# Kernel tuning notes

Measured on AMD Instinct MI355X. Metric: run time of the kernel, lower is better.

Reference implementation:

```python
import jax, jax.numpy as jnp
import numpy as np

B, S, D, H = 4, 2048, 1024, 16
DK = D // H
THETA = 10000.0


def setup_inputs() -> dict:
    key = jax.random.key(0)
    ks = jax.random.split(key, 5)
    std = (2.0 / (D + D)) ** 0.5  # Linear init std (distribution differs from trunc-normal; math identical)
    x = jax.random.normal(ks[0], (B, S, D), dtype=jnp.float32)
    wq = jax.random.normal(ks[1], (D, D), dtype=jnp.float32) * std
    wk = jax.random.normal(ks[2], (D, D), dtype=jnp.float32) * std
    wv = jax.random.normal(ks[3], (D, D), dtype=jnp.float32) * std
    wo = jax.random.normal(ks[4], (D, D), dtype=jnp.float32) * std
    mask = jnp.tril(jnp.ones((S, S), dtype=bool))  # causal
    return {"x": x, "mask": mask, "wq": wq, "wk": wk, "wv": wv, "wo": wo}


def _rope(t):
    # t: [b, h, s, dk]; interleaved pairs (even, odd)
    s = t.shape[-2]
    inv_freq = THETA ** (-jnp.arange(0, DK, 2, dtype=jnp.float32) / DK)  # [dk/2]
    ang = jnp.arange(s, dtype=jnp.float32)[:, None] * inv_freq[None, :]  # [s, dk/2]
    cos = jnp.cos(ang)[None, None, :, :]
    sin = jnp.sin(ang)[None, None, :, :]
    x1 = t[..., 0::2]
    x2 = t[..., 1::2]
    rot = jnp.stack([x1 * cos - x2 * sin, x1 * sin + x2 * cos], axis=-1)
    return rot.reshape(t.shape)


def reference(x, mask, wq, wk, wv, wo):
    b, s, d = x.shape
    def heads(w):
        return jnp.einsum('bsd,ed->bse', x, w).reshape(b, s, H, DK).transpose(0, 2, 1, 3)
    q = _rope(heads(wq))
    k = _rope(heads(wk))
    v = heads(wv)
    scores = jnp.einsum('bhqd,bhkd->bhqk', q, k) / (DK ** 0.5)
    scores = jnp.where(mask, scores, -jnp.inf)
    attn = jax.nn.softmax(scores, axis=-1)
    out = jnp.einsum('bhqk,bhkd->bhqd', attn, v)
    out = out.transpose(0, 2, 1, 3).reshape(b, s, d)
    return jnp.einsum('bsd,ed->bse', out, wo)
```

## Files before the change

kernel.cpp:

```cpp
#include <hip/hip_runtime.h>

constexpr int Bc = 4, Sc = 2048, Dc = 1024, Hc = 16, DKc = 64;
constexpr int Mc = Bc * Sc;

typedef __bf16 bf16x8 __attribute__((ext_vector_type(8)));
typedef float f32x4 __attribute__((ext_vector_type(4)));
typedef unsigned short ush;

#define DEVI __device__ __forceinline__

DEVI ush bf(float f) { return __builtin_bit_cast(ush, (__bf16)f); }

DEVI void ld_lds16(const void* g, void* l) {
    __builtin_amdgcn_global_load_lds(
        (const __attribute__((address_space(1))) unsigned int*)g,
        (__attribute__((address_space(3))) unsigned int*)l,
        16, 0, 0);
}

constexpr unsigned CVT_BLOCKS = 6144;
constexpr unsigned TAB_BLOCKS = 32;

__global__ __launch_bounds__(256) void cvt_all(
    const float* __restrict__ x,  const float* __restrict__ wq,
    const float* __restrict__ wk, const float* __restrict__ wv,
    const float* __restrict__ wo, ush* __restrict__ dst,
    float2* __restrict__ csn)
{
    if (blockIdx.x >= CVT_BLOCKS) {
        int t = (int)(blockIdx.x - CVT_BLOCKS) * 256 + threadIdx.x;
#pragma unroll
        for (int i = 0; i < 8; i++) {
            int idx = t * 8 + i;
            int s = idx >> 5, p = idx & 31;
            float ang = (float)s * exp2f(-(float)p * 0.4152410118609203f);
            csn[idx] = make_float2(cosf(ang), sinf(ang));
        }
        return;
    }
    size_t t = ((size_t)blockIdx.x * 256 + threadIdx.x) * 8;
    const float* src; size_t loc;
    const size_t NX = (size_t)Mc * Dc;
    if (t < NX) { src = x; loc = t; }
    else {
        size_t u = t - NX;
        int wi = (int)(u >> 20);
        src = (wi == 0) ? wq : ((wi == 1) ? wk : ((wi == 2) ? wv : wo));
        loc = u & 1048575u;
    }
    float4 a = *(const float4*)(src + loc);
    float4 b = *(const float4*)(src + loc + 4);
    union { ush u[8]; float4 v; } o;
    o.u[0] = bf(a.x); o.u[1] = bf(a.y); o.u[2] = bf(a.z); o.u[3] = bf(a.w);
    o.u[4] = bf(b.x); o.u[5] = bf(b.y); o.u[6] = bf(b.z); o.u[7] = bf(b.w);
    *(float4*)(dst + t) = o.v;
}

template<int MODE>
__global__ __launch_bounds__(512, 4) void gemm_bf(
    const ush* __restrict__ A,
    const ush* __restrict__ W0, const ush* __restrict__ W1,
    const ush* __restrict__ W2,
    ush* __restrict__ Oq, ush* __restrict__ Ok, ush* __restrict__ Ovt,
    float* __restrict__ Of, const float2* __restrict__ csn)
{
    __shared__ ush sA[128 * 64];
    __shared__ ush sB[128 * 64];

    const int xcd = (int)blockIdx.x;
    const int u = (int)blockIdx.y + 64 * (int)blockIdx.z;
    const int z = (MODE == 0) ? (u >> 6) : 0;
    const int w = u & 63;
    const int m0 = (xcd * 8 + (w >> 3)) * 128;
    const int n0 = (w & 7) * 128;

    const ush* W = (z == 0) ? W0 : ((z == 1) ? W1 : W2);

    const int tid = threadIdx.x;
    const int wv = tid >> 6;
    const int ln = tid & 63;
    const int lr = ln & 15;
    const int lq = ln >> 4;
    const int wm = (wv & 1) * 64;
    const int wn = (wv >> 1) * 32;
    const int rL = ln >> 3;
    const int cSw = ((ln & 7) ^ rL) * 8;
    const int ca0 = lq ^ (ln & 7);

    f32x4 acc[4][2] = {};
    const bool swp = (MODE == 0) && (z == 2);

    for (int kt = 0; kt < 1024; kt += 64) {
        __syncthreads();
#pragma unroll
        for (int i = 0; i < 2; i++) {
            int chunk = wv * 2 + i;
            int rr = chunk * 8 + rL;
            ld_lds16(&A[(size_t)(m0 + rr) * 1024 + kt + cSw], &sA[chunk * 512]);
            ld_lds16(&W[(size_t)(n0 + rr) * 1024 + kt + cSw], &sB[chunk * 512]);
        }
        __syncthreads();
#pragma unroll
        for (int ks = 0; ks < 2; ks++) {
            const int cf = (ca0 ^ (ks << 2)) << 3;
            bf16x8 af[4], bfr[2];
#pragma unroll
            for (int t = 0; t < 4; t++)
                af[t]  = *(const bf16x8*)(&sA[(wm + t * 16 + lr) * 64 + cf]);
#pragma unroll
            for (int t = 0; t < 2; t++)
                bfr[t] = *(const bf16x8*)(&sB[(wn + t * 16 + lr) * 64 + cf]);
            __builtin_amdgcn_s_setprio(1);
            if (!swp) {
#pragma unroll
                for (int ia = 0; ia < 4; ia++)
#pragma unroll
                    for (int ib = 0; ib < 2; ib++)
                        acc[ia][ib] = __builtin_amdgcn_mfma_f32_16x16x32_bf16(
                            af[ia], bfr[ib], acc[ia][ib], 0, 0, 0);
            } else {
#pragma unroll
                for (int ia = 0; ia < 4; ia++)
#pragma unroll
                    for (int ib = 0; ib < 2; ib++)
                        acc[ia][ib] = __builtin_amdgcn_mfma_f32_16x16x32_bf16(
                            bfr[ib], af[ia], acc[ia][ib], 0, 0, 0);
            }
            __builtin_amdgcn_s_setprio(0);
        }
    }

    ush* Oqk = (z == 0) ? Oq : Ok;
#pragma unroll
    for (int ia = 0; ia < 4; ia++) {
#pragma unroll
        for (int ib = 0; ib < 2; ib++) {
#pragma unroll
            for (int r = 0; r < 4; r++) {
                float v = acc[ia][ib][r];
                if (MODE == 1) {
                    int m = m0 + wm + ia * 16 + lq * 4 + r;
                    int n = n0 + wn + ib * 16 + lr;
                    Of[(size_t)m * 1024 + n] = v;
                } else if (swp) {
                    int n = n0 + wn + ib * 16 + lq * 4 + r;
                    int m = m0 + wm + ia * 16 + lr;
                    Ovt[((size_t)((m >> 11) * Hc + (n >> 6)) * DKc + (n & 63)) * Sc
                        + (m & (Sc - 1))] = bf(v);
                } else {
                    int m = m0 + wm + ia * 16 + lq * 4 + r;
                    int n = n0 + wn + ib * 16 + lr;
                    float part = __shfl_xor(v, 1);
                    int dk = n & 63, s = m & (Sc - 1);
                    float2 cs = csn[(s << 5) + (dk >> 1)];
                    float res = (dk & 1) ? (part * cs.y + v * cs.x)
                                         : (v * cs.x - part * cs.y);
                    if (z == 0) res *= 0.18033688011112042f;
                    Oqk[((size_t)((m >> 11) * Hc + (n >> 6)) * Sc + s) * DKc + dk] = bf(res);
                }
            }
        }
    }
}

__global__ __launch_bounds__(512, 4) void attn_k(
    const ush* __restrict__ Q, const ush* __restrict__ Kr,
    const ush* __restrict__ Vt, ush* __restrict__ O)
{
    __shared__ ush kbuf[2][64 * 64];
    __shared__ ush vbuf[2][64 * 64];
    __shared__ ush pbuf[8][16 * 76];

    const int head = (int)blockIdx.x * 8 + ((int)blockIdx.y >> 3);
    const int qp   = (int)blockIdx.y & 7;
    const int tid = threadIdx.x;
    const int wv = tid >> 6;
    const int ln = tid & 63;
    const int lr = ln & 15;
    const int lq = ln >> 4;
    const size_t hoff = (size_t)head * Sc * DKc;
    const int rS = tid >> 3;
    const int c8 = tid & 7;
    const int cS = c8 * 8;
    const int cW = ((c8 ^ (rS & 7)) * 8);
    const int cw0 = ((lq ^ (lr & 7)) * 8);

#define BARRIER() { asm volatile("s_waitcnt lgkmcnt(0)" ::: "memory");       \
        __builtin_amdgcn_sched_barrier(0);                                   \
        __builtin_amdgcn_s_barrier(); }

#define LOADKV(ktv, kk, vv) {                                                \
        int kb_ = (ktv) * 64;                                                \
        kk = *(const float4*)(&Kr[hoff + (size_t)(kb_ + rS) * DKc + cS]);    \
        vv = *(const float4*)(&Vt[hoff + (size_t)rS * Sc + kb_ + cS]); }

#define WRITEKV(bb, kk, vv) {                                                \
        *(float4*)(&kbuf[bb][rS * 64 + cW]) = kk;                            \
        *(float4*)(&vbuf[bb][rS * 64 + cW]) = vv; }

#define COMPUTE(bb, ktv) {                                                   \
        const int kb = (ktv) * 64;                                           \
        f32x4 sc[4];                                                         \
        __builtin_amdgcn_s_setprio(1);                                       \
        _Pragma("unroll")                                                    \
        for (int nt = 0; nt < 4; nt++) {                                     \
            const ush* kr_ = &kbuf[bb][(nt * 16 + lr) * 64];                 \
            bf16x8 bk0 = *(const bf16x8*)(kr_ + cw0);                        \
            bf16x8 bk1 = *(const bf16x8*)(kr_ + (cw0 ^ 32));                 \
            f32x4 cc = {};                                                   \
            cc = __builtin_amdgcn_mfma_f32_16x16x32_bf16(aq0, bk0, cc, 0, 0, 0); \
            cc = __builtin_amdgcn_mfma_f32_16x16x32_bf16(aq1, bk1, cc, 0, 0, 0); \
            sc[nt] = cc;                                                     \
        }                                                                    \
        __builtin_amdgcn_s_setprio(0);                                       \
        const int rowq = qbase + wv * 16 + lq * 4;                           \
        const bool needmask = (kb + 63 > qbase + wv * 16);                   \
        _Pragma("unroll")                                                    \
        for (int nt = 0; nt < 4; nt++) {                                     \
            int col = kb + nt * 16 + lr;                                     \
            _Pragma("unroll")                                                \
            for (int r = 0; r < 4; r++) {                                    \
                float v = sc[nt][r];                                         \
                if (needmask && col > rowq + r) v = -1e30f;                  \
                float p = exp2f(v);                                          \
                sc[nt][r] = p;                                               \
                rs[r] += p;                                                  \
            }                                                                \
        }                                                                    \
        {                                                                    \
            ush* pb = pbuf[wv];                                              \
            _Pragma("unroll")                                                \
            for (int nt = 0; nt < 4; nt++)                                   \
                _Pragma("unroll")                                            \
                for (int r = 0; r < 4; r++)                                  \
                    pb[(lq * 4 + r) * 76 + nt * 16 + lr] = bf(sc[nt][r]);    \
            __builtin_amdgcn_s_setprio(1);                                   \
            _Pragma("unroll")                                                \
            for (int ks = 0; ks < 2; ks++) {                                 \
                bf16x8 ap = *(const bf16x8*)(&pb[lr * 76 + ks * 32 + lq * 8]); \
                _Pragma("unroll")                                            \
                for (int nt = 0; nt < 4; nt++) {                             \
                    bf16x8 bv = *(const bf16x8*)(&vbuf[bb][(nt * 16 + lr) * 64 \
                                                       + (cw0 ^ (ks * 32))]); \
                    oacc[nt] = __builtin_amdgcn_mfma_f32_16x16x32_bf16(      \
                        ap, bv, oacc[nt], 0, 0, 0);                          \
                }                                                            \
            }                                                                \
            __builtin_amdgcn_s_setprio(0);                                   \
        }                                                                    \
    }

    for (int half = 0; half < 2; half++) {
        const int qt = half ? (15 - qp) : qp;
        const int qbase = qt * 128;
        const int kmax = 2 * qt + 2;

        bf16x8 aq0, aq1;
        {
            int row = qbase + wv * 16 + lr;
            const ush* qp_ = &Q[hoff + (size_t)row * DKc + lq * 8];
            aq0 = *(const bf16x8*)(qp_);
            aq1 = *(const bf16x8*)(qp_ + 32);
        }

        f32x4 oacc[4] = {};
        float rs[4] = {};

        float4 ka, va, kb2, vb2;

        LOADKV(0, ka, va);
        WRITEKV(0, ka, va);
        if (kmax > 1) LOADKV(1, kb2, vb2);
        BARRIER();

        int kt = 0;
        while (true) {
            if (kt + 1 < kmax) WRITEKV(1, kb2, vb2);
            if (kt + 2 < kmax) LOADKV(kt + 2, ka, va);
            COMPUTE(0, kt);
            BARRIER();
            kt++;
            if (kt >= kmax) break;
            if (kt + 1 < kmax) WRITEKV(0, ka, va);
            if (kt + 2 < kmax) LOADKV(kt + 2, kb2, vb2);
            COMPUTE(1, kt);
            BARRIER();
            kt++;
            if (kt >= kmax) break;
        }

        const int b = head >> 4, h = head & 15;
#pragma unroll
        for (int r = 0; r < 4; r++) {
            float l = rs[r];
#pragma unroll
            for (int d = 1; d < 16; d <<= 1) l += __shfl_xor(l, d);
            float inv = 1.0f / l;
            int srow = qbase + wv * 16 + lq * 4 + r;
#pragma unroll
            for (int nt = 0; nt < 4; nt++) {
                int e = h * 64 + nt * 16 + lr;
                O[((size_t)(b * Sc + srow)) * Dc + e] = bf(oacc[nt][r] * inv);
            }
        }
    }
#undef BARRIER
#undef LOADKV
#undef WRITEKV
#undef COMPUTE
}

extern "C" void kernel_launch(void* const* d_in, const int* in_sizes, int n_in,
                              void* d_out, int out_size, void* d_ws, size_t ws_size,
                              hipStream_t stream)
{
    (void)in_sizes; (void)n_in; (void)out_size; (void)ws_size;
    const float* x  = (const float*)d_in[0];
    const float* wq = (const float*)d_in[2];
    const float* wk = (const float*)d_in[3];
    const float* wv = (const float*)d_in[4];
    const float* wo = (const float*)d_in[5];

    const size_t N = (size_t)Mc * Dc;
    const size_t NW = (size_t)Dc * Dc;

    ush* xh  = (ush*)d_ws;
    ush* wqh = xh  + N;
    ush* wkh = wqh + NW;
    ush* wvh = wkh + NW;
    ush* woh = wvh + NW;
    ush* vt  = woh + NW;
    ush* ows = vt  + N;
    float2* csn = (float2*)(ows + N);
    ush* qd = (ush*)d_out;
    ush* kd = qd + N;

    cvt_all<<<dim3(CVT_BLOCKS + TAB_BLOCKS), 256, 0, stream>>>(
        x, wq, wk, wv, wo, xh, csn);
    gemm_bf<0><<<dim3(8, 64, 3), 512, 0, stream>>>(
        xh, wqh, wkh, wvh, qd, kd, vt, nullptr, csn);
    attn_k<<<dim3(8, 64), 512, 0, stream>>>(qd, kd, vt, ows);
    gemm_bf<1><<<dim3(8, 64, 1), 512, 0, stream>>>(
        ows, woh, woh, woh, nullptr, nullptr, nullptr, (float*)d_out, csn);
}
```

Baseline: 292.9 us.

## Transpose QK^T MFMA operands so each lane owns a query row

```diff
diff --git a/kernel.cpp b/kernel.cpp
--- a/kernel.cpp
+++ b/kernel.cpp
@@ -200,6 +200,7 @@
 
 #define COMPUTE(bb, ktv) {                                                   \
         const int kb = (ktv) * 64;                                           \
+        if (kb <= qbase + wv * 16 + 15) {       \
         f32x4 sc[4];                                                         \
         __builtin_amdgcn_s_setprio(1);                                       \
         _Pragma("unroll")                                                    \
@@ -208,32 +209,37 @@
             bf16x8 bk0 = *(const bf16x8*)(kr_ + cw0);                        \
             bf16x8 bk1 = *(const bf16x8*)(kr_ + (cw0 ^ 32));                 \
             f32x4 cc = {};                                                   \
-            cc = __builtin_amdgcn_mfma_f32_16x16x32_bf16(aq0, bk0, cc, 0, 0, 0); \
-            cc = __builtin_amdgcn_mfma_f32_16x16x32_bf16(aq1, bk1, cc, 0, 0, 0); \
+                    \
+            cc = __builtin_amdgcn_mfma_f32_16x16x32_bf16(bk0, aq0, cc, 0, 0, 0); \
+            cc = __builtin_amdgcn_mfma_f32_16x16x32_bf16(bk1, aq1, cc, 0, 0, 0); \
             sc[nt] = cc;                                                     \
         }                                                                    \
         __builtin_amdgcn_s_setprio(0);                                       \
-        const int rowq = qbase + wv * 16 + lq * 4;                           \
+                 \
+        const int qg = qbase + wv * 16 + lr;                                 \
         const bool needmask = (kb + 63 > qbase + wv * 16);                   \
         _Pragma("unroll")                                                    \
         for (int nt = 0; nt < 4; nt++) {                                     \
-            int col = kb + nt * 16 + lr;                                     \
+            int k0_ = kb + nt * 16 + lq * 4;                                 \
             _Pragma("unroll")                                                \
             for (int r = 0; r < 4; r++) {                                    \
                 float v = sc[nt][r];                                         \
-                if (needmask && col > rowq + r) v = -1e30f;                  \
+                if (needmask && (k0_ + r) > qg) v = -1e30f;                  \
                 float p = exp2f(v);                                          \
                 sc[nt][r] = p;                                               \
-                rs[r] += p;                                                  \
+                rs += p;                                                     \
             }                                                                \
         }                                                                    \
         {                                                                    \
             ush* pb = pbuf[wv];                                              \
+                    \
             _Pragma("unroll")                                                \
-            for (int nt = 0; nt < 4; nt++)                                   \
-                _Pragma("unroll")                                            \
-                for (int r = 0; r < 4; r++)                                  \
-                    pb[(lq * 4 + r) * 76 + nt * 16 + lr] = bf(sc[nt][r]);    \
+            for (int nt = 0; nt < 4; nt++) {                                 \
+                uint2 u_;                                                    \
+                u_.x = (unsigned)bf(sc[nt][0]) | ((unsigned)bf(sc[nt][1]) << 16); \
+                u_.y = (unsigned)bf(sc[nt][2]) | ((unsigned)bf(sc[nt][3]) << 16); \
+                *(uint2*)(&pb[lr * 76 + nt * 16 + lq * 4]) = u_;             \
+            }                                                                \
             __builtin_amdgcn_s_setprio(1);                                   \
             _Pragma("unroll")                                                \
             for (int ks = 0; ks < 2; ks++) {                                 \
@@ -248,7 +254,7 @@
             }                                                                \
             __builtin_amdgcn_s_setprio(0);                                   \
         }                                                                    \
-    }
+        } }
 
     for (int half = 0; half < 2; half++) {
         const int qt = half ? (15 - qp) : qp;
@@ -264,7 +270,7 @@
         }
 
         f32x4 oacc[4] = {};
-        float rs[4] = {};
+        float rs = 0.0f;
 
         float4 ka, va, kb2, vb2;
 
@@ -290,13 +296,15 @@
         }
 
         const int b = head >> 4, h = head & 15;
+        float l = rs;
+        l += __shfl_xor(l, 16);
+        l += __shfl_xor(l, 32);
 #pragma unroll
         for (int r = 0; r < 4; r++) {
-            float l = rs[r];
-#pragma unroll
-            for (int d = 1; d < 16; d <<= 1) l += __shfl_xor(l, d);
-            float inv = 1.0f / l;
-            int srow = qbase + wv * 16 + lq * 4 + r;
+            int q = lq * 4 + r;
+            float lsum = __shfl(l, (ln & 48) | q);
+            float inv = 1.0f / lsum;
+            int srow = qbase + wv * 16 + q;
 #pragma unroll
             for (int nt = 0; nt < 4; nt++) {
                 int e = h * 64 + nt * 16 + lr;
```

Result: faster. 275.7 us (median of 2 runs) (-5.9%).
